# Optimization experiments

Hardware: AMD Instinct MI355X
Metric: run time of the kernel (lower is better)

## Reference

```python
import jax, jax.numpy as jnp
import numpy as np

B, N_GLOBAL, D, E = 4096, 64, 256, 4
TPE = N_GLOBAL // E
EPS = 1e-5


def setup_inputs() -> dict:
    key = jax.random.key(0)
    ks = jax.random.split(key, 5)
    X_global = jax.random.normal(ks[0], (B, N_GLOBAL, D), dtype=jnp.float32)
    # per-expert deep MLP params: Linear(tpe*d -> d), Linear(d -> tpe*d)
    f = TPE * D
    W1 = jax.random.normal(ks[1], (E, f, D), dtype=jnp.float32) * (f ** -0.5)
    b1 = jax.random.normal(ks[2], (E, D), dtype=jnp.float32) * 0.01
    W2 = jax.random.normal(ks[3], (E, D, f), dtype=jnp.float32) * (D ** -0.5)
    b2 = jax.random.normal(ks[4], (E, f), dtype=jnp.float32) * 0.01
    gamma = jnp.ones((E, D), dtype=jnp.float32)
    beta = jnp.zeros((E, D), dtype=jnp.float32)
    return {"X_global": X_global, "W1": W1, "b1": b1, "W2": W2, "b2": b2,
            "gamma": gamma, "beta": beta}


def reference(X_global, W1, b1, W2, b2, gamma, beta):
    Bn, n_global, d = X_global.shape
    e = W1.shape[0]
    tpe = n_global // e
    scale = d ** -0.5
    # static partition: (B, E, tpe, d)
    Xp = X_global.reshape(Bn, e, tpe, d)
    # DOT-product self-attention per expert partition
    scores = jnp.einsum('bend,bemd->benm', Xp, Xp) * scale  # (B,E,tpe,tpe)
    X_dot = jnp.einsum('benm,bemd->bend', jax.nn.softmax(scores, axis=-1), Xp)
    # deep MLP on flattened partition
    Xf = Xp.reshape(Bn, e, tpe * d)
    h = jax.nn.relu(jnp.einsum('bef,efh->beh', Xf, W1) + b1[None])  # (B,E,d)
    X_deep = (jnp.einsum('beh,ehf->bef', h, W2) + b2[None]).reshape(Bn, e, tpe, d)
    # residual + LayerNorm over last dim (biased variance, eps=1e-5)
    Y = X_dot + X_deep + Xp
    mu = jnp.mean(Y, axis=-1, keepdims=True)
    var = jnp.mean(jnp.square(Y - mu), axis=-1, keepdims=True)
    Yn = (Y - mu) * jax.lax.rsqrt(var + EPS)
    Yn = Yn * gamma[None, :, None, :] + beta[None, :, None, :]
    return Yn.reshape(Bn, n_global, d)
```

## Files before the change

### kernel.cpp

```cpp
#include <hip/hip_runtime.h>


typedef __attribute__((ext_vector_type(4))) float f32x4;
typedef __bf16 bf16;
typedef __attribute__((ext_vector_type(8))) bf16 bf16x8;
typedef __attribute__((ext_vector_type(4))) bf16 bf16x4;
typedef __attribute__((ext_vector_type(2))) bf16 bf16x2;

#define DEV static __device__ __forceinline__

DEV f32x4 zero4() { return f32x4{0.f, 0.f, 0.f, 0.f}; }

DEV bf16x8 cvt8(const f32x4& a, const f32x4& b) {
  bf16x8 o;
  o[0] = (bf16)a.x; o[1] = (bf16)a.y; o[2] = (bf16)a.z; o[3] = (bf16)a.w;
  o[4] = (bf16)b.x; o[5] = (bf16)b.y; o[6] = (bf16)b.z; o[7] = (bf16)b.w;
  return o;
}

__global__ __launch_bounds__(256) void pack_w1(const float* __restrict__ W1,
                                               bf16* __restrict__ P) {
  const int e = blockIdx.z, kc = blockIdx.y;
  const int nf = blockIdx.x * 4 + (threadIdx.x >> 6);
  const int l = threadIdx.x & 63;
  const float* src = W1 + (size_t)e * 4096 * 256 +
                     (size_t)(kc * 32 + (l >> 4) * 8) * 256 + nf * 16 + (l & 15);
  bf16x8 o;
#pragma unroll
  for (int j = 0; j < 8; j++) o[j] = (bf16)src[(size_t)j * 256];
  *(bf16x8*)&P[(((size_t)e * 128 + kc) * 16 + nf) * 512 + l * 8] = o;
}

__global__ __launch_bounds__(256) void pack_w2(const float* __restrict__ W2,
                                               bf16* __restrict__ P) {
  const int e = blockIdx.z, t = blockIdx.y, kc = blockIdx.x;
  const int l = threadIdx.x & 63;
#pragma unroll
  for (int it = 0; it < 4; it++) {
    int nfl = it * 4 + (threadIdx.x >> 6);
    const float* src = W2 + (size_t)e * 256 * 4096 +
                       (size_t)(kc * 32 + (l >> 4) * 8) * 4096 + t * 256 +
                       nfl * 16 + (l & 15);
    bf16x8 o;
#pragma unroll
    for (int j = 0; j < 8; j++) o[j] = (bf16)src[(size_t)j * 4096];
    *(bf16x8*)&P[(((size_t)e * 256 + t * 16 + nfl) * 8 + kc) * 512 + l * 8] = o;
  }
}

__global__ __launch_bounds__(256) void fused_ag(
    const float* __restrict__ X, const bf16* __restrict__ W1P,
    const float* __restrict__ b1, float* __restrict__ Y0f,
    bf16* __restrict__ Y0b, bf16* __restrict__ HP, int useBf) {
  __shared__ __align__(16) bf16 S[4 * 4608];
  __shared__ __align__(16) bf16 Plw[4 * 256];
  __shared__ __align__(16) bf16 Zb[8];
  const int tid = threadIdx.x, lane = tid & 63, w = tid >> 6;
  const int lr = lane & 15, g = lane >> 4;
  const int fid = blockIdx.x;
  const int sub = fid & 511;
  const int e = (sub & 7) >> 1;
  const int m = ((sub >> 3) << 1) | (sub & 1);
  const int b0 = m * 32;

  if (fid < 512) {
    bf16* xt = &S[w * 4608];
    bf16* plw = &Plw[w * 256];
    if (tid < 8) Zb[tid] = (bf16)0.f;
    __syncthreads();
    const int koff = (g & 1) * 8;

    f32x4 raw[16];
    {
      const float* Xb = X + (size_t)(b0 + w) * 16384 + e * 4096;
#pragma unroll
      for (int c = 0; c < 8; c++) {
        const float* qq = Xb + lr * 256 + c * 32 + g * 8;
        raw[2 * c] = *(const f32x4*)qq;
        raw[2 * c + 1] = *(const f32x4*)(qq + 4);
      }
    }

    for (int q = 0; q < 8; q++) {
      const int bp = b0 + q * 4 + w;
      const size_t obase0 = (size_t)bp * 16384 + e * 4096;

      bf16x8 af[8];
#pragma unroll
      for (int c = 0; c < 8; c++) {
        bf16x8 o = cvt8(raw[2 * c], raw[2 * c + 1]);
        af[c] = o;
#pragma unroll
        for (int j = 0; j < 8; j++)
          xt[(c * 32 + g * 8 + j) * 18 + lr] = o[j];
      }

      f32x4 s = zero4();
#pragma unroll
      for (int c = 0; c < 8; c++)
        s = __builtin_amdgcn_mfma_f32_16x16x32_bf16(af[c], af[c], s, 0, 0, 0);

      if (q < 7) {
        const float* Xb = X + (size_t)(bp + 4) * 16384 + e * 4096;
#pragma unroll
        for (int c = 0; c < 8; c++) {
          const float* qq = Xb + lr * 256 + c * 32 + g * 8;
          raw[2 * c] = *(const f32x4*)qq;
          raw[2 * c + 1] = *(const f32x4*)(qq + 4);
        }
      }

      float pv[4];
#pragma unroll
      for (int r = 0; r < 4; r++) {
        float v = s[r] * 0.0625f;
        float mx = v;
#pragma unroll
        for (int mm = 1; mm < 16; mm <<= 1) mx = fmaxf(mx, __shfl_xor(mx, mm));
        float ev = __expf(v - mx);
        float sum = ev;
#pragma unroll
        for (int mm = 1; mm < 16; mm <<= 1) sum += __shfl_xor(sum, mm);
        pv[r] = ev / sum + ((lr == g * 4 + r) ? 1.0f : 0.0f);
      }
#pragma unroll
      for (int r = 0; r < 4; r++) plw[(g * 4 + r) * 16 + lr] = (bf16)pv[r];
      const bf16* psrc = (g < 2) ? &plw[lr * 16 + g * 8] : &Zb[0];
      bf16x8 pf = *(const bf16x8*)psrc;

      float yo[16][4];
#pragma unroll
      for (int nc = 0; nc < 16; nc++) {
        const bf16* rowp = &xt[(nc * 16 + lr) * 18];
        bf16x8 bfr;
#pragma unroll
        for (int h = 0; h < 4; h++) {
          bf16x2 tv = *(const bf16x2*)&rowp[koff + h * 2];
          bfr[2 * h] = tv[0];
          bfr[2 * h + 1] = tv[1];
        }
        f32x4 xd =
            __builtin_amdgcn_mfma_f32_16x16x32_bf16(pf, bfr, zero4(), 0, 0, 0);
        yo[nc][0] = xd[0];
        yo[nc][1] = xd[1];
        yo[nc][2] = xd[2];
        yo[nc][3] = xd[3];
      }

#pragma unroll
      for (int nc = 0; nc < 16; nc++)
#pragma unroll
        for (int r = 0; r < 4; r++)
          xt[(g * 4 + r) * 268 + nc * 16 + lr] = (bf16)yo[nc][r];

      const int tok = lane >> 2, cc = lane & 3;
      if (useBf) {
#pragma unroll
        for (int i = 0; i < 8; i++) {
          int d0 = i * 32 + cc * 8;
          bf16x4 v0 = *(const bf16x4*)&xt[tok * 268 + d0];
          bf16x4 v1 = *(const bf16x4*)&xt[tok * 268 + d0 + 4];
          bf16x8 v;
          v[0] = v0[0]; v[1] = v0[1]; v[2] = v0[2]; v[3] = v0[3];
          v[4] = v1[0]; v[5] = v1[1]; v[6] = v1[2]; v[7] = v1[3];
          *(bf16x8*)&Y0b[obase0 + tok * 256 + d0] = v;
        }
      } else {
#pragma unroll
        for (int i = 0; i < 8; i++) {
          int d0 = i * 32 + cc * 8;
          bf16x4 v0 = *(const bf16x4*)&xt[tok * 268 + d0];
          bf16x4 v1 = *(const bf16x4*)&xt[tok * 268 + d0 + 4];
          f32x4 a, bb;
          a.x = (float)v0[0]; a.y = (float)v0[1];
          a.z = (float)v0[2]; a.w = (float)v0[3];
          bb.x = (float)v1[0]; bb.y = (float)v1[1];
          bb.z = (float)v1[2]; bb.w = (float)v1[3];
          *(f32x4*)&Y0f[obase0 + tok * 256 + d0] = a;
          *(f32x4*)&Y0f[obase0 + tok * 256 + d0 + 4] = bb;
        }
      }
    }
  } else {
    bf16* Ab0 = S;
    bf16* Ab1 = S + 4352;
    const int arow = tid >> 3, ak0 = (tid & 7) * 16;
    const size_t abase = (size_t)(b0 + arow) * 16384 + e * 4096 + ak0;
    const bf16* Wp = W1P + (size_t)e * 128 * 16 * 512;

    f32x4 acc[2][4];
#pragma unroll
    for (int i = 0; i < 2; i++)
#pragma unroll
      for (int j = 0; j < 4; j++) acc[i][j] = zero4();

    f32x4 p0, p1, p2, p3;
    {
      const float* q = X + abase;
      p0 = *(const f32x4*)q;       p1 = *(const f32x4*)(q + 4);
      p2 = *(const f32x4*)(q + 8); p3 = *(const f32x4*)(q + 12);
    }

    for (int kt = 0; kt < 32; kt++) {
      bf16* Ac = (kt & 1) ? Ab1 : Ab0;
      *(bf16x8*)&Ac[arow * 136 + ak0] = cvt8(p0, p1);
      *(bf16x8*)&Ac[arow * 136 + ak0 + 8] = cvt8(p2, p3);
      if (kt < 31) {
        const float* q = X + abase + (kt + 1) * 128;
        p0 = *(const f32x4*)q;       p1 = *(const f32x4*)(q + 4);
        p2 = *(const f32x4*)(q + 8); p3 = *(const f32x4*)(q + 12);
      }
      __syncthreads();
#pragma unroll
      for (int kki = 0; kki < 4; kki++) {
        const int kc = kt * 4 + kki;
        bf16x8 afr[2], bfr[4];
#pragma unroll
        for (int i = 0; i < 2; i++)
          afr[i] = *(const bf16x8*)&Ac[(i * 16 + lr) * 136 + kki * 32 + g * 8];
#pragma unroll
        for (int j = 0; j < 4; j++)
          bfr[j] = *(const bf16x8*)&Wp[(((size_t)kc) * 16 + w * 4 + j) * 512 +
                                       lane * 8];
#pragma unroll
        for (int i = 0; i < 2; i++)
#pragma unroll
          for (int j = 0; j < 4; j++)
            acc[i][j] = __builtin_amdgcn_mfma_f32_16x16x32_bf16(
                afr[i], bfr[j], acc[i][j], 0, 0, 0);
      }
    }
#pragma unroll
    for (int j = 0; j < 4; j++) {
      const int col = w * 64 + j * 16 + lr;
      const float bv = b1[e * 256 + col];
      const int kc = col >> 5, lhi = (col >> 3) & 3, jj = col & 7;
#pragma unroll
      for (int i = 0; i < 2; i++) {
        const int mfg = m * 2 + i;
        bf16* dst = HP + (((size_t)e * 256 + mfg) * 8 + kc) * 512 + jj;
#pragma unroll
        for (int r = 0; r < 4; r++) {
          float v = fmaxf(acc[i][j][r] + bv, 0.f);
          dst[(lhi * 16 + g * 4 + r) * 8] = (bf16)v;
        }
      }
    }
  }
}

__global__ __launch_bounds__(512) void gemm2_kernel(
    const bf16* __restrict__ HP, const bf16* __restrict__ W2P,
    const float* __restrict__ b2, const float* __restrict__ gamma,
    const float* __restrict__ beta, const float* __restrict__ Y0f,
    const bf16* __restrict__ Y0b, int useBf, float* __restrict__ Out) {
  __shared__ __align__(16) bf16 T[64 * 264];
  const int fid = blockIdx.x;
  const int e = fid & 3;
  const int rr_ = fid >> 2;
  const int t = rr_ & 15;
  const int ms = rr_ >> 4;
  const int tid = threadIdx.x, lane = tid & 63, w = tid >> 6;
  const int lr = lane & 15, g = lane >> 4;
  const int erow = tid >> 3, ec = tid & 7;

  bf16x8 breg[2][8];
  {
    const bf16* Wp = W2P + (((size_t)e * 256 + t * 16 + w * 2) * 8) * 512 +
                     lane * 8;
#pragma unroll
    for (int nj = 0; nj < 2; nj++)
#pragma unroll
      for (int kc = 0; kc < 8; kc++)
        breg[nj][kc] = *(const bf16x8*)&Wp[(size_t)(nj * 8 + kc) * 512];
  }
  float b2v[2];
#pragma unroll
  for (int nj = 0; nj < 2; nj++)
    b2v[nj] = b2[e * 4096 + t * 256 + w * 32 + nj * 16 + lr];

  for (int it = 0; it < 2; it++) {
    const int mt = ms * 2 + it;
    const int b0 = mt * 64;
    const size_t ebase =
        (size_t)(b0 + erow) * 16384 + e * 4096 + t * 256 + ec * 32;

    bf16x8 y0r[4];
    if (useBf) {
#pragma unroll
      for (int u = 0; u < 4; u++)
        y0r[u] = *(const bf16x8*)&Y0b[ebase + u * 8];
    }

    const bf16* Ap = HP + (((size_t)e * 256 + mt * 4) * 8) * 512 + lane * 8;
    f32x4 acc[4][2];
#pragma unroll
    for (int mf = 0; mf < 4; mf++)
#pragma unroll
      for (int nj = 0; nj < 2; nj++) acc[mf][nj] = zero4();

    bf16x8 afr[4], afn[4];
#pragma unroll
    for (int mf = 0; mf < 4; mf++)
      afr[mf] = *(const bf16x8*)&Ap[(size_t)(mf * 8) * 512];
#pragma unroll
    for (int kc = 0; kc < 8; kc++) {
      if (kc < 7) {
#pragma unroll
        for (int mf = 0; mf < 4; mf++)
          afn[mf] = *(const bf16x8*)&Ap[(size_t)(mf * 8 + kc + 1) * 512];
      }
#pragma unroll
      for (int mf = 0; mf < 4; mf++)
#pragma unroll
        for (int nj = 0; nj < 2; nj++)
          acc[mf][nj] = __builtin_amdgcn_mfma_f32_16x16x32_bf16(
              afr[mf], breg[nj][kc], acc[mf][nj], 0, 0, 0);
#pragma unroll
      for (int mf = 0; mf < 4; mf++) afr[mf] = afn[mf];
    }

    __syncthreads();
#pragma unroll
    for (int mf = 0; mf < 4; mf++)
#pragma unroll
      for (int nj = 0; nj < 2; nj++)
#pragma unroll
        for (int r = 0; r < 4; r++)
          T[(mf * 16 + g * 4 + r) * 264 + w * 32 + nj * 16 + lr] =
              (bf16)(acc[mf][nj][r] + b2v[nj]);
    __syncthreads();

    float y[4][8];
    float s1 = 0.f, s2 = 0.f;
#pragma unroll
    for (int u = 0; u < 4; u++) {
      bf16x8 tv = *(const bf16x8*)&T[erow * 264 + ec * 32 + u * 8];
      if (useBf) {
#pragma unroll
        for (int u8 = 0; u8 < 8; u8++) {
          float v = (float)tv[u8] + (float)y0r[u][u8];
          y[u][u8] = v;
          s1 += v;
          s2 += v * v;
        }
      } else {
        f32x4 a = *(const f32x4*)&Y0f[ebase + u * 8];
        f32x4 bb = *(const f32x4*)&Y0f[ebase + u * 8 + 4];
#pragma unroll
        for (int u8 = 0; u8 < 8; u8++) {
          float v = (float)tv[u8] + (u8 < 4 ? a[u8] : bb[u8 - 4]);
          y[u][u8] = v;
          s1 += v;
          s2 += v * v;
        }
      }
    }
    s1 += __shfl_xor(s1, 1); s1 += __shfl_xor(s1, 2); s1 += __shfl_xor(s1, 4);
    s2 += __shfl_xor(s2, 1); s2 += __shfl_xor(s2, 2); s2 += __shfl_xor(s2, 4);
    const float mu = s1 * (1.f / 256.f);
    const float var = s2 * (1.f / 256.f) - mu * mu;
    const float rs = rsqrtf(var + 1e-5f);

#pragma unroll
    for (int u = 0; u < 4; u++) {
      const int col = ec * 32 + u * 8;
      f32x4 gv0 = *(const f32x4*)&gamma[e * 256 + col];
      f32x4 gv1 = *(const f32x4*)&gamma[e * 256 + col + 4];
      f32x4 bt0 = *(const f32x4*)&beta[e * 256 + col];
      f32x4 bt1 = *(const f32x4*)&beta[e * 256 + col + 4];
      f32x4 o0, o1;
#pragma unroll
      for (int u8 = 0; u8 < 4; u8++) {
        o0[u8] = (y[u][u8] - mu) * rs * gv0[u8] + bt0[u8];
        o1[u8] = (y[u][u8 + 4] - mu) * rs * gv1[u8] + bt1[u8];
      }
      *(f32x4*)&Out[ebase + u * 8] = o0;
      *(f32x4*)&Out[ebase + u * 8 + 4] = o1;
    }
  }
}

extern "C" void kernel_launch(void* const* d_in, const int* in_sizes, int n_in,
                              void* d_out, int out_size, void* d_ws, size_t ws_size,
                              hipStream_t stream) {
  const float* X     = (const float*)d_in[0];
  const float* W1    = (const float*)d_in[1];
  const float* b1    = (const float*)d_in[2];
  const float* W2    = (const float*)d_in[3];
  const float* b2    = (const float*)d_in[4];
  const float* gamma = (const float*)d_in[5];
  const float* beta  = (const float*)d_in[6];
  float* Out = (float*)d_out;

  const size_t MB8 = (size_t)4 * 1048576;
  bf16* W1P = (bf16*)d_ws;
  bf16* W2P = W1P + MB8;
  bf16* HP  = W2P + MB8;
  bf16* Y0b = HP + MB8;

  const size_t bigN = (size_t)4096 * 16384 * 2;
  const size_t base = 3 * (MB8 * 2);
  const int useBf = (ws_size >= base + bigN) ? 1 : 0;

  pack_w1<<<dim3(4, 128, 4), dim3(256), 0, stream>>>(W1, W1P);
  pack_w2<<<dim3(8, 16, 4), dim3(256), 0, stream>>>(W2, W2P);
  fused_ag<<<dim3(1024), dim3(256), 0, stream>>>(X, W1P, b1, Out, Y0b, HP, useBf);
  gemm2_kernel<<<dim3(2048), dim3(512), 0, stream>>>(HP, W2P, b2, gamma, beta,
                                                     Out, Y0b, useBf, Out);
}
```

Baseline: 405.4 us.

## Split attention work into one partition per wave and launch GEMM blocks first

The attention branch of the fused kernel no longer loops over eight (batch, expert) partitions per wave with register prefetch. Each wave now handles a single partition, and the grid grows from 1024 to 4608 blocks. The GEMM1 blocks take the first 512 block indices so they are dispatched before the many short attention blocks. This aims to expose more parallelism and balance load across CUs, at the cost of more block launches and dropping the software prefetch of the next partition's X.

```diff
diff --git a/kernel.cpp b/kernel.cpp
--- a/kernel.cpp
+++ b/kernel.cpp
@@ -58,130 +58,112 @@
   const int tid = threadIdx.x, lane = tid & 63, w = tid >> 6;
   const int lr = lane & 15, g = lane >> 4;
   const int fid = blockIdx.x;
-  const int sub = fid & 511;
-  const int e = (sub & 7) >> 1;
-  const int m = ((sub >> 3) << 1) | (sub & 1);
-  const int b0 = m * 32;
-
-  if (fid < 512) {
+
+  if (fid >= 512) {
     bf16* xt = &S[w * 4608];
     bf16* plw = &Plw[w * 256];
     if (tid < 8) Zb[tid] = (bf16)0.f;
     __syncthreads();
     const int koff = (g & 1) * 8;
 
-    f32x4 raw[16];
-    {
-      const float* Xb = X + (size_t)(b0 + w) * 16384 + e * 4096;
-#pragma unroll
-      for (int c = 0; c < 8; c++) {
-        const float* qq = Xb + lr * 256 + c * 32 + g * 8;
-        raw[2 * c] = *(const f32x4*)qq;
-        raw[2 * c + 1] = *(const f32x4*)(qq + 4);
-      }
-    }
-
-    for (int q = 0; q < 8; q++) {
-      const int bp = b0 + q * 4 + w;
-      const size_t obase0 = (size_t)bp * 16384 + e * 4096;
-
-      bf16x8 af[8];
-#pragma unroll
-      for (int c = 0; c < 8; c++) {
-        bf16x8 o = cvt8(raw[2 * c], raw[2 * c + 1]);
-        af[c] = o;
-#pragma unroll
-        for (int j = 0; j < 8; j++)
-          xt[(c * 32 + g * 8 + j) * 18 + lr] = o[j];
-      }
-
-      f32x4 s = zero4();
-#pragma unroll
-      for (int c = 0; c < 8; c++)
-        s = __builtin_amdgcn_mfma_f32_16x16x32_bf16(af[c], af[c], s, 0, 0, 0);
-
-      if (q < 7) {
-        const float* Xb = X + (size_t)(bp + 4) * 16384 + e * 4096;
-#pragma unroll
-        for (int c = 0; c < 8; c++) {
-          const float* qq = Xb + lr * 256 + c * 32 + g * 8;
-          raw[2 * c] = *(const f32x4*)qq;
-          raw[2 * c + 1] = *(const f32x4*)(qq + 4);
-        }
-      }
-
-      float pv[4];
-#pragma unroll
-      for (int r = 0; r < 4; r++) {
-        float v = s[r] * 0.0625f;
-        float mx = v;
-#pragma unroll
-        for (int mm = 1; mm < 16; mm <<= 1) mx = fmaxf(mx, __shfl_xor(mx, mm));
-        float ev = __expf(v - mx);
-        float sum = ev;
-#pragma unroll
-        for (int mm = 1; mm < 16; mm <<= 1) sum += __shfl_xor(sum, mm);
-        pv[r] = ev / sum + ((lr == g * 4 + r) ? 1.0f : 0.0f);
-      }
-#pragma unroll
-      for (int r = 0; r < 4; r++) plw[(g * 4 + r) * 16 + lr] = (bf16)pv[r];
-      const bf16* psrc = (g < 2) ? &plw[lr * 16 + g * 8] : &Zb[0];
-      bf16x8 pf = *(const bf16x8*)psrc;
-
-      float yo[16][4];
-#pragma unroll
-      for (int nc = 0; nc < 16; nc++) {
-        const bf16* rowp = &xt[(nc * 16 + lr) * 18];
-        bf16x8 bfr;
-#pragma unroll
-        for (int h = 0; h < 4; h++) {
-          bf16x2 tv = *(const bf16x2*)&rowp[koff + h * 2];
-          bfr[2 * h] = tv[0];
-          bfr[2 * h + 1] = tv[1];
-        }
-        f32x4 xd =
-            __builtin_amdgcn_mfma_f32_16x16x32_bf16(pf, bfr, zero4(), 0, 0, 0);
-        yo[nc][0] = xd[0];
-        yo[nc][1] = xd[1];
-        yo[nc][2] = xd[2];
-        yo[nc][3] = xd[3];
-      }
-
-#pragma unroll
-      for (int nc = 0; nc < 16; nc++)
-#pragma unroll
-        for (int r = 0; r < 4; r++)
-          xt[(g * 4 + r) * 268 + nc * 16 + lr] = (bf16)yo[nc][r];
-
-      const int tok = lane >> 2, cc = lane & 3;
-      if (useBf) {
-#pragma unroll
-        for (int i = 0; i < 8; i++) {
-          int d0 = i * 32 + cc * 8;
-          bf16x4 v0 = *(const bf16x4*)&xt[tok * 268 + d0];
-          bf16x4 v1 = *(const bf16x4*)&xt[tok * 268 + d0 + 4];
-          bf16x8 v;
-          v[0] = v0[0]; v[1] = v0[1]; v[2] = v0[2]; v[3] = v0[3];
-          v[4] = v1[0]; v[5] = v1[1]; v[6] = v1[2]; v[7] = v1[3];
-          *(bf16x8*)&Y0b[obase0 + tok * 256 + d0] = v;
-        }
-      } else {
-#pragma unroll
-        for (int i = 0; i < 8; i++) {
-          int d0 = i * 32 + cc * 8;
-          bf16x4 v0 = *(const bf16x4*)&xt[tok * 268 + d0];
-          bf16x4 v1 = *(const bf16x4*)&xt[tok * 268 + d0 + 4];
-          f32x4 a, bb;
-          a.x = (float)v0[0]; a.y = (float)v0[1];
-          a.z = (float)v0[2]; a.w = (float)v0[3];
-          bb.x = (float)v1[0]; bb.y = (float)v1[1];
-          bb.z = (float)v1[2]; bb.w = (float)v1[3];
-          *(f32x4*)&Y0f[obase0 + tok * 256 + d0] = a;
-          *(f32x4*)&Y0f[obase0 + tok * 256 + d0 + 4] = bb;
-        }
+    const int p = (fid - 512) * 4 + w;
+    const int b = p >> 2, e = p & 3;
+    const size_t obase0 = (size_t)b * 16384 + e * 4096;
+    const float* Xb = X + obase0;
+
+    bf16x8 af[8];
+#pragma unroll
+    for (int c = 0; c < 8; c++) {
+      const float* qq = Xb + lr * 256 + c * 32 + g * 8;
+      f32x4 v0 = *(const f32x4*)qq;
+      f32x4 v1 = *(const f32x4*)(qq + 4);
+      bf16x8 o = cvt8(v0, v1);
+      af[c] = o;
+#pragma unroll
+      for (int j = 0; j < 8; j++)
+        xt[(c * 32 + g * 8 + j) * 18 + lr] = o[j];
+    }
+
+    f32x4 s = zero4();
+#pragma unroll
+    for (int c = 0; c < 8; c++)
+      s = __builtin_amdgcn_mfma_f32_16x16x32_bf16(af[c], af[c], s, 0, 0, 0);
+
+    float pv[4];
+#pragma unroll
+    for (int r = 0; r < 4; r++) {
+      float v = s[r] * 0.0625f;
+      float mx = v;
+#pragma unroll
+      for (int mm = 1; mm < 16; mm <<= 1) mx = fmaxf(mx, __shfl_xor(mx, mm));
+      float ev = __expf(v - mx);
+      float sum = ev;
+#pragma unroll
+      for (int mm = 1; mm < 16; mm <<= 1) sum += __shfl_xor(sum, mm);
+      pv[r] = ev / sum + ((lr == g * 4 + r) ? 1.0f : 0.0f);
+    }
+#pragma unroll
+    for (int r = 0; r < 4; r++) plw[(g * 4 + r) * 16 + lr] = (bf16)pv[r];
+    const bf16* psrc = (g < 2) ? &plw[lr * 16 + g * 8] : &Zb[0];
+    bf16x8 pf = *(const bf16x8*)psrc;
+
+    float yo[16][4];
+#pragma unroll
+    for (int nc = 0; nc < 16; nc++) {
+      const bf16* rowp = &xt[(nc * 16 + lr) * 18];
+      bf16x8 bfr;
+#pragma unroll
+      for (int h = 0; h < 4; h++) {
+        bf16x2 tv = *(const bf16x2*)&rowp[koff + h * 2];
+        bfr[2 * h] = tv[0];
+        bfr[2 * h + 1] = tv[1];
+      }
+      f32x4 xd =
+          __builtin_amdgcn_mfma_f32_16x16x32_bf16(pf, bfr, zero4(), 0, 0, 0);
+      yo[nc][0] = xd[0];
+      yo[nc][1] = xd[1];
+      yo[nc][2] = xd[2];
+      yo[nc][3] = xd[3];
+    }
+
+#pragma unroll
+    for (int nc = 0; nc < 16; nc++)
+#pragma unroll
+      for (int r = 0; r < 4; r++)
+        xt[(g * 4 + r) * 268 + nc * 16 + lr] = (bf16)yo[nc][r];
+
+    const int tok = lane >> 2, cc = lane & 3;
+    if (useBf) {
+#pragma unroll
+      for (int i = 0; i < 8; i++) {
+        int d0 = i * 32 + cc * 8;
+        bf16x4 v0 = *(const bf16x4*)&xt[tok * 268 + d0];
+        bf16x4 v1 = *(const bf16x4*)&xt[tok * 268 + d0 + 4];
+        bf16x8 v;
+        v[0] = v0[0]; v[1] = v0[1]; v[2] = v0[2]; v[3] = v0[3];
+        v[4] = v1[0]; v[5] = v1[1]; v[6] = v1[2]; v[7] = v1[3];
+        *(bf16x8*)&Y0b[obase0 + tok * 256 + d0] = v;
+      }
+    } else {
+#pragma unroll
+      for (int i = 0; i < 8; i++) {
+        int d0 = i * 32 + cc * 8;
+        bf16x4 v0 = *(const bf16x4*)&xt[tok * 268 + d0];
+        bf16x4 v1 = *(const bf16x4*)&xt[tok * 268 + d0 + 4];
+        f32x4 a, bb;
+        a.x = (float)v0[0]; a.y = (float)v0[1];
+        a.z = (float)v0[2]; a.w = (float)v0[3];
+        bb.x = (float)v1[0]; bb.y = (float)v1[1];
+        bb.z = (float)v1[2]; bb.w = (float)v1[3];
+        *(f32x4*)&Y0f[obase0 + tok * 256 + d0] = a;
+        *(f32x4*)&Y0f[obase0 + tok * 256 + d0 + 4] = bb;
       }
     }
   } else {
+    const int sub = fid;
+    const int e = (sub & 7) >> 1;
+    const int m = ((sub >> 3) << 1) | (sub & 1);
+    const int b0 = m * 32;
     bf16* Ab0 = S;
     bf16* Ab1 = S + 4352;
     const int arow = tid >> 3, ak0 = (tid & 7) * 16;
@@ -405,7 +387,7 @@
 
   pack_w1<<<dim3(4, 128, 4), dim3(256), 0, stream>>>(W1, W1P);
   pack_w2<<<dim3(8, 16, 4), dim3(256), 0, stream>>>(W2, W2P);
-  fused_ag<<<dim3(1024), dim3(256), 0, stream>>>(X, W1P, b1, Out, Y0b, HP, useBf);
+  fused_ag<<<dim3(4608), dim3(256), 0, stream>>>(X, W1P, b1, Out, Y0b, HP, useBf);
   gemm2_kernel<<<dim3(2048), dim3(512), 0, stream>>>(HP, W2P, b2, gamma, beta,
                                                      Out, Y0b, useBf, Out);
 }
```

Result: faster. 369.0 us (-9.0%).
